# Optimization experiments

Hardware: AMD Instinct MI355X
Metric: run time of the kernel (lower is better)

## Reference

```python
import jax, jax.numpy as jnp
import numpy as np

HEADS = 16
TARGET_TOKENS = 128  # deterministic choice of image_tokens (original picks randomly from [729,128])


def _1d_sincos(embed_dim, pos):
    omega = np.arange(embed_dim // 2, dtype=np.float32)
    omega /= embed_dim / 2.0
    omega = 1.0 / 10000 ** omega
    out = np.einsum('m,d->md', pos.reshape(-1), omega)
    return np.concatenate([np.sin(out), np.cos(out)], axis=1)


def spatial_pos_embed(embed_dim, grid_size):
    d_sp = embed_dim // 4 * 3
    gh = np.arange(grid_size, dtype=np.float32)
    grid = np.stack(np.meshgrid(gh, gh), axis=0).reshape([2, 1, grid_size, grid_size])
    emb = np.concatenate([_1d_sincos(d_sp // 2, grid[0]), _1d_sincos(d_sp // 2, grid[1])], axis=1)
    emb = emb[np.newaxis]
    pad = np.zeros((1, emb.shape[1], embed_dim - d_sp), dtype=np.float32)
    return np.concatenate([pad, emb], axis=-1).reshape(1, grid_size * grid_size, embed_dim)


def setup_inputs() -> dict:
    key = jax.random.key(0)
    ks = jax.random.split(key, 4)
    B, P, C, H = 64, 729, 1152, 3584
    x = jax.random.normal(ks[0], (B, P, C), jnp.float32)
    w1 = jax.random.normal(ks[1], (C, H), jnp.float32) * (1.0 / np.sqrt(C))
    b1 = jnp.zeros((H,), jnp.float32)
    w2 = jax.random.normal(ks[2], (H, H), jnp.float32) * (1.0 / np.sqrt(H))
    b2 = jnp.zeros((H,), jnp.float32)
    spatial_pos = jnp.asarray(spatial_pos_embed(C, 27))
    return {'x': x, 'spatial_pos': spatial_pos, 'w1': w1, 'b1': b1,
            'w2': w2, 'b2': b2, 'local_num_frames': 1}


def _match_indices(metric, r):
    # ToMe bipartite soft matching: metric [B, T, d]
    metric = metric / jnp.linalg.norm(metric, axis=-1, keepdims=True)
    a, b = metric[:, ::2], metric[:, 1::2]
    scores = jnp.einsum('bic,bjc->bij', a, b)   # [B, Ta, Tb]
    node_max = scores.max(-1)
    node_idx = scores.argmax(-1)
    edge_idx = jnp.argsort(-node_max, axis=-1)
    unm_idx = edge_idx[:, r:]                    # kept src tokens
    src_idx = edge_idx[:, :r]                    # merged src tokens
    dst_idx = jnp.take_along_axis(node_idx, src_idx, axis=-1)
    return unm_idx, src_idx, dst_idx


def _merge_sum(x, unm_idx, src_idx, dst_idx):
    src, dst = x[:, ::2], x[:, 1::2]
    unm = jnp.take_along_axis(src, unm_idx[:, :, None], axis=1)
    sel = jnp.take_along_axis(src, src_idx[:, :, None], axis=1)
    dst = jax.vmap(lambda d, i, v: d.at[i].add(v))(dst, dst_idx, sel)
    return jnp.concatenate([unm, dst], axis=1)


def merge_tokens(x, target, heads):
    b, p, c = x.shape
    if p == target:
        return x
    rs, tmp = [], p
    while tmp != target:
        if tmp - target <= tmp // 2:
            rs.append(tmp - target)
            break
        rs.append(tmp // 2)
        tmp -= tmp // 2
    size = jnp.ones((b, p, 1), x.dtype)
    for r in rs:  # static schedule, e.g. [364, 182, 55]
        t = x.shape[1]
        metric = x.reshape(b, t, heads, c // heads).mean(2)
        idxs = _match_indices(metric, r)
        x = _merge_sum(x * size, *idxs)
        size = _merge_sum(size, *idxs)
        x = x / size
    return x


def reference(x, spatial_pos, w1, b1, w2, b2, local_num_frames):
    # is_image=True path
    x = x + spatial_pos
    x = merge_tokens(x, TARGET_TOKENS, HEADS)
    h = jax.nn.gelu(jnp.einsum('bpc,ch->bph', x, w1) + b1, approximate=False)
    return jnp.einsum('bph,ho->bpo', h, w2) + b2
```

## Files before the change

### kernel.cpp

```cpp
#include <hip/hip_runtime.h>
#include <hip/hip_bf16.h>
#include <stdint.h>

#define BB 64
#define P0 729
#define CC 1152
#define HD 72
#define NHEAD 16
#define HH 3584
#define TT 128
#define NSTR 365
#define SCB 384
#define MAXCB 6

typedef __hip_bfloat16 bf16;
typedef unsigned short u16;
typedef __attribute__((ext_vector_type(8))) short short8;
typedef __attribute__((ext_vector_type(4))) float floatx4;

__device__ inline u16 f2bf(float v) {
  bf16 h = __float2bfloat16(v);
  return *(u16*)&h;
}

__device__ inline void load_lds16(const void* g, void* l) {
  __builtin_amdgcn_global_load_lds(
      (const __attribute__((address_space(1))) uint32_t*)g,
      (__attribute__((address_space(3))) uint32_t*)l, 16, 0, 0);
}

__global__ __launch_bounds__(128)
void k_init(const float* __restrict__ x, const float* __restrict__ pos,
            double* __restrict__ mo, int* __restrict__ amap) {
  __shared__ float xs[CC], ps[CC];
  int bp = blockIdx.x;
  int p = bp % P0;
  int tid = threadIdx.x;
  const float4* xr = (const float4*)(x + (size_t)bp * CC);
  const float4* pr = (const float4*)(pos + (size_t)p * CC);
  for (int idx = tid; idx < CC / 4; idx += 128) {
    ((float4*)xs)[idx] = xr[idx];
    ((float4*)ps)[idx] = pr[idx];
  }
  __syncthreads();
  if (tid < HD) {
    double s = 0.0;
    #pragma unroll
    for (int h = 0; h < NHEAD; ++h) {
      int c = h * HD + tid;
      s += (double)xs[c] + (double)ps[c];
    }
    mo[(size_t)bp * HD + tid] = s * (1.0 / 16.0);
  }
  if (tid == 0) amap[bp] = p;
}

__global__ void k_rnorm(const double* __restrict__ m, double* __restrict__ rn, int t) {
  int bi = blockIdx.x;
  int lane = threadIdx.x;
  const double* row = m + (size_t)bi * HD;
  double v = 0.0;
  if (lane < HD) { double a = row[lane]; v = a * a; }
  if (lane < HD - 64) { double a = row[lane + 64]; v += a * a; }
  for (int off = 32; off; off >>= 1) v += __shfl_down(v, off, 64);
  if (lane == 0) {
    int b = bi / t, i = bi % t;
    rn[b * P0 + i] = 1.0 / sqrt(v);
  }
}

__global__ __launch_bounds__(256)
void k_score2(const double* __restrict__ m, const double* __restrict__ rn,
              double* __restrict__ pmax, int* __restrict__ pidx,
              int t, int s, int d) {
  __shared__ double sL[64][37];
  __shared__ double sD[64][37];
  int b = blockIdx.z;
  int i0 = blockIdx.x * 64, j0 = blockIdx.y * 64;
  int tid = threadIdx.x;
  int tx = tid & 15, ty = tid >> 4;
  double acc[4][4] = {};
  for (int kc = 0; kc < HD; kc += 36) {
    for (int idx = tid; idx < 64 * 36; idx += 256) {
      int row = idx / 36, k = idx - row * 36;
      int i = i0 + row;
      sL[row][k] = (i < s) ? m[((size_t)b * t + 2 * i) * HD + kc + k] : 0.0;
      int j = j0 + row;
      sD[row][k] = (j < d) ? m[((size_t)b * t + 2 * j + 1) * HD + kc + k] : 0.0;
    }
    __syncthreads();
    #pragma unroll 6
    for (int k = 0; k < 36; ++k) {
      double la[4], ld[4];
      #pragma unroll
      for (int a = 0; a < 4; ++a) la[a] = sL[ty + 16 * a][k];
      #pragma unroll
      for (int c = 0; c < 4; ++c) ld[c] = sD[tx + 16 * c][k];
      #pragma unroll
      for (int a = 0; a < 4; ++a)
        #pragma unroll
        for (int c = 0; c < 4; ++c)
          acc[a][c] += la[a] * ld[c];
    }
    __syncthreads();
  }
  #pragma unroll
  for (int a = 0; a < 4; ++a) {
    int i = i0 + ty + 16 * a;
    double rni = (i < s) ? rn[b * P0 + 2 * i] : 0.0;
    double best = -1e300; int bj = 0x7fffffff;
    #pragma unroll
    for (int c = 0; c < 4; ++c) {
      int j = j0 + tx + 16 * c;
      double sc = (j < d) ? acc[a][c] * rni * rn[b * P0 + 2 * j + 1] : -1e300;
      if (sc > best) { best = sc; bj = j; }
    }
    for (int off = 8; off; off >>= 1) {
      double ov = __shfl_down(best, off, 16);
      int oj = __shfl_down(bj, off, 16);
      if (ov > best || (ov == best && oj < bj)) { best = ov; bj = oj; }
    }
    if (tx == 0 && i < s) {
      pmax[((size_t)b * MAXCB + blockIdx.y) * SCB + i] = best;
      pidx[((size_t)b * MAXCB + blockIdx.y) * SCB + i] = bj;
    }
  }
}

__global__ void k_colred(const double* __restrict__ pmax, const int* __restrict__ pidx,
                         double* __restrict__ nmax, int* __restrict__ nidx,
                         int s, int ncb) {
  int b = blockIdx.x, i = threadIdx.x;
  if (i >= s) return;
  double best = -1e300; int bj = 0x7fffffff;
  for (int cb = 0; cb < ncb; ++cb) {
    double v = pmax[((size_t)b * MAXCB + cb) * SCB + i];
    int j = pidx[((size_t)b * MAXCB + cb) * SCB + i];
    if (v > best) { best = v; bj = j; }
  }
  nmax[b * NSTR + i] = best; nidx[b * NSTR + i] = bj;
}

template <int SZ>
__global__ __launch_bounds__(512)
void k_sort(const double* __restrict__ nmax, int* __restrict__ eidx, int s) {
  __shared__ double v[SZ];
  __shared__ int ix[SZ];
  int b = blockIdx.x, tid = threadIdx.x;
  if (tid < s) { v[tid] = nmax[b * NSTR + tid]; ix[tid] = tid; }
  else { v[tid] = -1e308; ix[tid] = 1024 + tid; }
  __syncthreads();
  for (int k = 2; k <= SZ; k <<= 1)
    for (int j = k >> 1; j > 0; j >>= 1) {
      int l = tid ^ j;
      if (l > tid) {
        double va = v[tid], vb = v[l]; int ia = ix[tid], ib = ix[l];
        bool b_before_a = (vb > va) || (vb == va && ib < ia);
        bool a_before_b = (va > vb) || (va == vb && ia < ib);
        bool dir = ((tid & k) == 0);
        bool sw = dir ? b_before_a : a_before_b;
        if (sw) { v[tid] = vb; v[l] = va; ix[tid] = ib; ix[l] = ia; }
      }
      __syncthreads();
    }
  if (tid < s) eidx[b * NSTR + tid] = ix[tid];
}

__global__ __launch_bounds__(512)
void k_mapround(const int* __restrict__ eidx, const int* __restrict__ nidx,
                int* __restrict__ amap, int t, int s, int r, int unm) {
  __shared__ int pos_of[NSTR];
  __shared__ int rmap[P0];
  int b = blockIdx.x, tid = threadIdx.x;
  for (int q = tid; q < s; q += 512) pos_of[eidx[b * NSTR + q]] = q;
  __syncthreads();
  for (int j = tid; j < t; j += 512) {
    int nm;
    if (j & 1) {
      nm = unm + (j >> 1);
    } else {
      int i = j >> 1;
      int q = pos_of[i];
      nm = (q >= r) ? (q - r)
                    : (unm + nidx[b * NSTR + i]);
    }
    rmap[j] = nm;
  }
  __syncthreads();
  for (int p = tid; p < P0; p += 512) {
    int cur = amap[b * P0 + p];
    amap[b * P0 + p] = rmap[cur];
  }
}

__global__ void k_gather_d(const double* __restrict__ mo, double* __restrict__ mn,
                           const int* __restrict__ eidx,
                           int t, int r, int unm, int tnew) {
  size_t idx = (size_t)blockIdx.x * 256 + threadIdx.x;
  size_t total = (size_t)BB * tnew * HD;
  if (idx >= total) return;
  int k = idx % HD;
  int o = (idx / HD) % tnew;
  int b = idx / ((size_t)HD * tnew);
  int tok = (o < unm) ? 2 * eidx[b * NSTR + r + o] : 2 * (o - unm) + 1;
  mn[idx] = mo[((size_t)b * t + tok) * HD + k];
}

__global__ void k_scatter_d(const double* __restrict__ mo, double* __restrict__ mn,
                            const int* __restrict__ eidx, const int* __restrict__ nidx,
                            int t, int r, int unm, int tnew) {
  size_t idx = (size_t)blockIdx.x * 256 + threadIdx.x;
  size_t total = (size_t)BB * r * HD;
  if (idx >= total) return;
  int k = idx % HD;
  int q = (idx / HD) % r;
  int b = idx / ((size_t)HD * r);
  int si = eidx[b * NSTR + q];
  int di = nidx[b * NSTR + si];
  atomicAdd(&mn[((size_t)b * tnew + unm + di) * HD + k],
            mo[((size_t)b * t + 2 * si) * HD + k]);
}

__global__ __launch_bounds__(256)
void k_buildcsr(const int* __restrict__ amap, int* __restrict__ sizes,
                int* __restrict__ offs, int* __restrict__ list) {
  __shared__ int cnt[TT], off_s[TT], cur[TT];
  int b = blockIdx.x, tid = threadIdx.x;
  if (tid < TT) { cnt[tid] = 0; cur[tid] = 0; }
  __syncthreads();
  for (int p = tid; p < P0; p += 256) atomicAdd(&cnt[amap[b * P0 + p]], 1);
  __syncthreads();
  if (tid == 0) {
    int acc = 0;
    for (int o = 0; o < TT; ++o) { off_s[o] = acc; acc += cnt[o]; }
  }
  __syncthreads();
  if (tid < TT) { sizes[b * TT + tid] = cnt[tid]; offs[b * TT + tid] = off_s[tid]; }
  for (int p = tid; p < P0; p += 256) {
    int o = amap[b * P0 + p];
    int pos = atomicAdd(&cur[o], 1);
    list[b * P0 + off_s[o] + pos] = p;
  }
}

__global__ __launch_bounds__(256)
void k_assemble(const float* __restrict__ x, const float* __restrict__ pos,
                const int* __restrict__ sizes, const int* __restrict__ offs,
                const int* __restrict__ list, bf16* __restrict__ xb) {
  __shared__ int ml[P0];
  int o = blockIdx.x, b = blockIdx.y, tid = threadIdx.x;
  int n = sizes[b * TT + o];
  int off = offs[b * TT + o];
  for (int i = tid; i < n; i += 256) ml[i] = list[b * P0 + off + i];
  __syncthreads();
  const int C4 = CC / 4;
  const bool two = (tid < C4 - 256);
  float4 a0 = {0.f, 0.f, 0.f, 0.f}, a1 = {0.f, 0.f, 0.f, 0.f};
  int i = 0;
  for (; i + 4 <= n; i += 4) {
    int p0 = ml[i], p1 = ml[i + 1], p2 = ml[i + 2], p3 = ml[i + 3];
    const float4* x0 = (const float4*)(x + ((size_t)b * P0 + p0) * CC);
    const float4* x1 = (const float4*)(x + ((size_t)b * P0 + p1) * CC);
    const float4* x2 = (const float4*)(x + ((size_t)b * P0 + p2) * CC);
    const float4* x3 = (const float4*)(x + ((size_t)b * P0 + p3) * CC);
    const float4* q0 = (const float4*)(pos + (size_t)p0 * CC);
    const float4* q1 = (const float4*)(pos + (size_t)p1 * CC);
    const float4* q2 = (const float4*)(pos + (size_t)p2 * CC);
    const float4* q3 = (const float4*)(pos + (size_t)p3 * CC);
    float4 v0 = x0[tid], v1 = x1[tid], v2 = x2[tid], v3 = x3[tid];
    float4 w0 = q0[tid], w1 = q1[tid], w2 = q2[tid], w3 = q3[tid];
    a0.x += (v0.x + w0.x) + (v1.x + w1.x) + (v2.x + w2.x) + (v3.x + w3.x);
    a0.y += (v0.y + w0.y) + (v1.y + w1.y) + (v2.y + w2.y) + (v3.y + w3.y);
    a0.z += (v0.z + w0.z) + (v1.z + w1.z) + (v2.z + w2.z) + (v3.z + w3.z);
    a0.w += (v0.w + w0.w) + (v1.w + w1.w) + (v2.w + w2.w) + (v3.w + w3.w);
    if (two) {
      float4 u0 = x0[tid + 256], u1 = x1[tid + 256], u2 = x2[tid + 256], u3 = x3[tid + 256];
      float4 s0 = q0[tid + 256], s1 = q1[tid + 256], s2 = q2[tid + 256], s3 = q3[tid + 256];
      a1.x += (u0.x + s0.x) + (u1.x + s1.x) + (u2.x + s2.x) + (u3.x + s3.x);
      a1.y += (u0.y + s0.y) + (u1.y + s1.y) + (u2.y + s2.y) + (u3.y + s3.y);
      a1.z += (u0.z + s0.z) + (u1.z + s1.z) + (u2.z + s2.z) + (u3.z + s3.z);
      a1.w += (u0.w + s0.w) + (u1.w + s1.w) + (u2.w + s2.w) + (u3.w + s3.w);
    }
  }
  for (; i < n; ++i) {
    int p = ml[i];
    const float4* xr = (const float4*)(x + ((size_t)b * P0 + p) * CC);
    const float4* pr = (const float4*)(pos + (size_t)p * CC);
    float4 v = xr[tid], w = pr[tid];
    a0.x += v.x + w.x; a0.y += v.y + w.y; a0.z += v.z + w.z; a0.w += v.w + w.w;
    if (two) {
      float4 v1 = xr[tid + 256], w1 = pr[tid + 256];
      a1.x += v1.x + w1.x; a1.y += v1.y + w1.y; a1.z += v1.z + w1.z; a1.w += v1.w + w1.w;
    }
  }
  float inv = 1.0f / (float)n;
  bf16* orow = xb + ((size_t)b * TT + o) * CC;
  ushort4 pk;
  pk.x = f2bf(a0.x * inv);
  pk.y = f2bf(a0.y * inv);
  pk.z = f2bf(a0.z * inv);
  pk.w = f2bf(a0.w * inv);
  ((ushort4*)orow)[tid] = pk;
  if (two) {
    ushort4 pk1;
    pk1.x = f2bf(a1.x * inv);
    pk1.y = f2bf(a1.y * inv);
    pk1.z = f2bf(a1.z * inv);
    pk1.w = f2bf(a1.w * inv);
    ((ushort4*)orow)[tid + 256] = pk1;
  }
}

__global__ void k_transpose(const float* __restrict__ w, bf16* __restrict__ wt,
                            int K, int N) {
  __shared__ float tile[32][33];
  int n0 = blockIdx.x * 32, k0 = blockIdx.y * 32;
  int tx = threadIdx.x, ty = threadIdx.y;
  #pragma unroll
  for (int yy = 0; yy < 32; yy += 8)
    tile[ty + yy][tx] = w[(size_t)(k0 + ty + yy) * N + n0 + tx];
  __syncthreads();
  #pragma unroll
  for (int yy = 0; yy < 32; yy += 8)
    wt[(size_t)(n0 + ty + yy) * K + k0 + tx] = __float2bfloat16(tile[tx][ty + yy]);
}


#define SBAR __builtin_amdgcn_sched_barrier(0)

#define STAGE_A(BUF, HHF, KT) do {                                        \
    int ktc_ = (KT) < nkt ? (KT) : nkt - 1;                               \
    const u16* s_ = gA + (size_t)(HHF) * 128 * K + ktc_ * 64;             \
    u16* d_ = dA + (BUF) * 16384 + (HHF) * 8192;                          \
    load_lds16(s_, d_);                                                   \
    load_lds16(s_ + (size_t)64 * K, d_ + 4096);                           \
  } while (0)

#define STAGE_B(BUF, HHF, KT) do {                                        \
    int ktc_ = (KT) < nkt ? (KT) : nkt - 1;                               \
    const u16* s_ = gB + (size_t)(HHF) * 128 * K + ktc_ * 64;             \
    u16* d_ = dB + (BUF) * 16384 + (HHF) * 8192;                          \
    load_lds16(s_, d_);                                                   \
    load_lds16(s_ + (size_t)64 * K, d_ + 4096);                           \
  } while (0)

#define LOADA(QA) do {                                                    \
    _Pragma("unroll")                                                     \
    for (int f_ = 0; f_ < 4; ++f_) {                                      \
      const u16* p_ = Ab + ((QA) * 128 + wr64 + f_ * 16 + lrow) * 64;     \
      af[f_][0] = *(const short8*)(p_ + swo0);                            \
      af[f_][1] = *(const short8*)(p_ + swo1);                            \
    }                                                                     \
  } while (0)

#define LOADB(QB) do {                                                    \
    _Pragma("unroll")                                                     \
    for (int g_ = 0; g_ < 2; ++g_) {                                      \
      const u16* p_ = Bb + ((QB) * 128 + wc32 + g_ * 16 + lrow) * 64;     \
      bfr[g_][0] = *(const short8*)(p_ + swo0);                           \
      bfr[g_][1] = *(const short8*)(p_ + swo1);                           \
    }                                                                     \
  } while (0)

#define DO_MFMA(QA, QB) do {                                              \
    _Pragma("unroll")                                                     \
    for (int ks_ = 0; ks_ < 2; ++ks_)                                     \
      _Pragma("unroll")                                                   \
      for (int f_ = 0; f_ < 4; ++f_)                                      \
        _Pragma("unroll")                                                 \
        for (int g_ = 0; g_ < 2; ++g_)                                    \
          acc[QA][QB][f_][g_] = __builtin_amdgcn_mfma_f32_16x16x32_bf16(  \
              af[f_][ks_], bfr[g_][ks_], acc[QA][QB][f_][g_], 0, 0, 0);   \
  } while (0)

#define MIDBAR() do {                                                     \
    SBAR;                                                                 \
    __builtin_amdgcn_s_barrier();                                         \
    asm volatile("s_waitcnt lgkmcnt(0)" ::: "memory");                    \
    SBAR;                                                                 \
    __builtin_amdgcn_s_setprio(1);                                        \
  } while (0)

#define ENDBAR() do {                                                     \
    __builtin_amdgcn_s_setprio(0);                                        \
    SBAR;                                                                 \
    __builtin_amdgcn_s_barrier();                                         \
    SBAR;                                                                 \
  } while (0)

#define ENDBAR_VM() do {                                                  \
    __builtin_amdgcn_s_setprio(0);                                        \
    SBAR;                                                                 \
    asm volatile("s_waitcnt vmcnt(6)" ::: "memory");                      \
    SBAR;                                                                 \
    __builtin_amdgcn_s_barrier();                                         \
    SBAR;                                                                 \
  } while (0)

template <int EPI>
__global__ __launch_bounds__(512, 2)
void k_gemm(const u16* __restrict__ A, const u16* __restrict__ Bt,
            const float* __restrict__ bias, void* __restrict__ Cout,
            int M, int N, int K) {
  __shared__ u16 sAall[32768];
  __shared__ u16 sBall[32768];
  (void)M;
  const int tid = threadIdx.x;
  const int m0 = blockIdx.y * 256, n0 = blockIdx.x * 256;
  const int wave = tid >> 6, lane = tid & 63;
  const int wr64 = (wave >> 2) * 64;
  const int wc32 = (wave & 3) * 32;
  const int quad = lane >> 4, lrow = lane & 15;
  const int sw = lrow & 7;
  const int swo0 = ((quad ^ sw)) << 3;
  const int swo1 = (((quad | 4) ^ sw)) << 3;
  const int nkt = K >> 6;

  const int r = tid >> 3;
  const int c16 = (tid & 7) ^ (r & 7);
  const u16* gA = A + (size_t)(m0 + r) * K + c16 * 8;
  const u16* gB = Bt + (size_t)(n0 + r) * K + c16 * 8;
  u16* dA = sAall + (tid << 3);
  u16* dB = sBall + (tid << 3);

  floatx4 acc[2][2][4][2] = {};
  short8 af[4][2], bfr[2][2];

  STAGE_A(0, 0, 0); STAGE_B(0, 1, 0); STAGE_A(0, 1, 0); STAGE_B(0, 0, 0);
  STAGE_A(1, 0, 1); STAGE_B(1, 1, 1); STAGE_A(1, 1, 1);
  SBAR;
  asm volatile("s_waitcnt vmcnt(6)" ::: "memory");
  SBAR;
  __builtin_amdgcn_s_barrier();
  SBAR;

  for (int t = 0; t < nkt; ++t) {
    const int bb = t & 1;
    const u16* Ab = sAall + bb * 16384;
    const u16* Bb = sBall + bb * 16384;
    LOADA(0); LOADB(0);
    STAGE_B(bb ^ 1, 0, t + 1);
    MIDBAR(); DO_MFMA(0, 0); ENDBAR();
    LOADB(1);
    STAGE_A(bb, 0, t + 2);
    MIDBAR(); DO_MFMA(0, 1); ENDBAR();
    LOADA(1);
    STAGE_B(bb, 1, t + 2);
    MIDBAR(); DO_MFMA(1, 1); ENDBAR();
    LOADB(0);
    STAGE_A(bb, 1, t + 2);
    MIDBAR(); DO_MFMA(1, 0); ENDBAR_VM();
  }

  #pragma unroll
  for (int qb = 0; qb < 2; ++qb)
    #pragma unroll
    for (int g = 0; g < 2; ++g) {
      int col = n0 + qb * 128 + wc32 + g * 16 + lrow;
      float bc = bias[col];
      #pragma unroll
      for (int qa = 0; qa < 2; ++qa)
        #pragma unroll
        for (int f = 0; f < 4; ++f)
          #pragma unroll
          for (int rg = 0; rg < 4; ++rg) {
            int row = m0 + qa * 128 + wr64 + f * 16 + quad * 4 + rg;
            float v = acc[qa][qb][f][g][rg] + bc;
            if (EPI == 0) {
              float gl = 0.5f * v * (1.0f + erff(v * 0.70710678118654752f));
              ((bf16*)Cout)[(size_t)row * N + col] = __float2bfloat16(gl);
            } else {
              ((float*)Cout)[(size_t)row * N + col] = v;
            }
          }
    }
}

extern "C" void kernel_launch(void* const* d_in, const int* in_sizes, int n_in,
                              void* d_out, int out_size, void* d_ws, size_t ws_size,
                              hipStream_t stream) {
  const float* x   = (const float*)d_in[0];
  const float* pos = (const float*)d_in[1];
  const float* w1  = (const float*)d_in[2];
  const float* b1  = (const float*)d_in[3];
  const float* w2  = (const float*)d_in[4];
  const float* b2  = (const float*)d_in[5];

  uint8_t* wsp = (uint8_t*)d_ws;
  size_t off = 0;
  auto alloc = [&](size_t bytes) -> void* {
    void* p = wsp + off;
    off += (bytes + 255) & ~(size_t)255;
    return p;
  };
  double* m_a  = (double*)alloc((size_t)BB * P0 * HD * 8);
  double* m_b  = (double*)alloc((size_t)BB * NSTR * HD * 8);
  double* rn   = (double*)alloc((size_t)BB * P0 * 8);
  double* nmax = (double*)alloc((size_t)BB * NSTR * 8);
  int*    nidx = (int*)alloc((size_t)BB * NSTR * 4);
  int*    eidx = (int*)alloc((size_t)BB * NSTR * 4);
  double* pmax = (double*)alloc((size_t)BB * MAXCB * SCB * 8);
  int*    pidx = (int*)alloc((size_t)BB * MAXCB * SCB * 4);
  int*    amap = (int*)alloc((size_t)BB * P0 * 4);
  int*    szs  = (int*)alloc((size_t)BB * TT * 4);
  int*    offs = (int*)alloc((size_t)BB * TT * 4);
  int*    list = (int*)alloc((size_t)BB * P0 * 4);
  bf16*   xb   = (bf16*)alloc((size_t)BB * TT * CC * 2);
  bf16*   w1t  = (bf16*)alloc((size_t)HH * CC * 2);
  bf16*   w2t  = (bf16*)alloc((size_t)HH * HH * 2);
  bf16*   hb   = (bf16*)alloc((size_t)BB * TT * HH * 2);

  k_init<<<BB * P0, 128, 0, stream>>>(x, pos, m_a, amap);
  dim3 tb(32, 8);
  k_transpose<<<dim3(HH / 32, CC / 32), tb, 0, stream>>>(w1, w1t, CC, HH);
  k_transpose<<<dim3(HH / 32, HH / 32), tb, 0, stream>>>(w2, w2t, HH, HH);

  struct Rnd { int t, s, d, r, unm, tnew; };
  const Rnd R[3] = {{729, 365, 364, 364, 1, 365},
                    {365, 183, 182, 182, 1, 183},
                    {183,  92,  91,  55, 37, 128}};
  double* msrc[3] = {m_a, m_b, m_a};
  double* mdst[3] = {m_b, m_a, m_b};

  for (int rr = 0; rr < 3; ++rr) {
    Rnd q = R[rr];
    k_rnorm<<<BB * q.t, 64, 0, stream>>>(msrc[rr], rn, q.t);
    int rt = (q.s + 63) / 64, ct = (q.d + 63) / 64;
    dim3 sg(rt, ct, BB);
    k_score2<<<sg, 256, 0, stream>>>(msrc[rr], rn, pmax, pidx, q.t, q.s, q.d);
    k_colred<<<BB, 512, 0, stream>>>(pmax, pidx, nmax, nidx, q.s, ct);
    if (rr == 0)      k_sort<512><<<BB, 512, 0, stream>>>(nmax, eidx, q.s);
    else if (rr == 1) k_sort<256><<<BB, 256, 0, stream>>>(nmax, eidx, q.s);
    else              k_sort<128><<<BB, 128, 0, stream>>>(nmax, eidx, q.s);
    k_mapround<<<BB, 512, 0, stream>>>(eidx, nidx, amap, q.t, q.s, q.r, q.unm);
    if (rr < 2) {
      size_t tg = (size_t)BB * q.tnew * HD;
      k_gather_d<<<(tg + 255) / 256, 256, 0, stream>>>(msrc[rr], mdst[rr], eidx, q.t, q.r, q.unm, q.tnew);
      size_t ts = (size_t)BB * q.r * HD;
      k_scatter_d<<<(ts + 255) / 256, 256, 0, stream>>>(msrc[rr], mdst[rr], eidx, nidx, q.t, q.r, q.unm, q.tnew);
    }
  }

  k_buildcsr<<<BB, 256, 0, stream>>>(amap, szs, offs, list);
  k_assemble<<<dim3(TT, BB), 256, 0, stream>>>(x, pos, szs, offs, list, xb);

  k_gemm<0><<<dim3(HH / 256, (BB * TT) / 256), 512, 0, stream>>>(
      (const u16*)xb, (const u16*)w1t, b1, hb, BB * TT, HH, CC);
  k_gemm<1><<<dim3(HH / 256, (BB * TT) / 256), 512, 0, stream>>>(
      (const u16*)hb, (const u16*)w2t, b2, d_out, BB * TT, HH, HH);
}
```

Before: 1.204 ms.

## Double-buffer MFMA fragments across phases and swizzle workgroups per XCD

The GEMM main loop now keeps two register sets for the A and B fragments. The next A fragment is prefetched from the other LDS buffer while the current phase's MFMAs run, and the lgkmcnt waits are relaxed to partial counts so LDS reads overlap compute. Workgroup IDs are also remapped so consecutive tiles land on the same XCD, which should improve L2 reuse. The extra fragment registers raise register pressure under the 512x2 launch bounds, and the reworked waits carry a risk of subtle ordering hazards.

Result: faster. 1.124 ms (-6.7%).

```diff
diff --git a/kernel.cpp b/kernel.cpp
--- a/kernel.cpp
+++ b/kernel.cpp
@@ -344,25 +344,25 @@
     load_lds16(s_ + (size_t)64 * K, d_ + 4096);                           \
   } while (0)
 
-#define LOADA(QA) do {                                                    \
+#define LOAD_A(DST, BUF, QA) do {                                        \
     _Pragma("unroll")                                                     \
     for (int f_ = 0; f_ < 4; ++f_) {                                      \
-      const u16* p_ = Ab + ((QA) * 128 + wr64 + f_ * 16 + lrow) * 64;     \
-      af[f_][0] = *(const short8*)(p_ + swo0);                            \
-      af[f_][1] = *(const short8*)(p_ + swo1);                            \
+      const u16* p_ = (BUF) + ((QA) * 128 + wr64 + f_ * 16 + lrow) * 64;  \
+      DST[f_][0] = *(const short8*)(p_ + swo0);                           \
+      DST[f_][1] = *(const short8*)(p_ + swo1);                           \
     }                                                                     \
   } while (0)
 
-#define LOADB(QB) do {                                                    \
+#define LOAD_B(DST, BUF, QB) do {                                        \
     _Pragma("unroll")                                                     \
     for (int g_ = 0; g_ < 2; ++g_) {                                      \
-      const u16* p_ = Bb + ((QB) * 128 + wc32 + g_ * 16 + lrow) * 64;     \
-      bfr[g_][0] = *(const short8*)(p_ + swo0);                           \
-      bfr[g_][1] = *(const short8*)(p_ + swo1);                           \
+      const u16* p_ = (BUF) + ((QB) * 128 + wc32 + g_ * 16 + lrow) * 64;  \
+      DST[g_][0] = *(const short8*)(p_ + swo0);                           \
+      DST[g_][1] = *(const short8*)(p_ + swo1);                           \
     }                                                                     \
   } while (0)
 
-#define DO_MFMA(QA, QB) do {                                              \
+#define DO_MFMA(AF, BF, QA, QB) do {                                      \
     _Pragma("unroll")                                                     \
     for (int ks_ = 0; ks_ < 2; ++ks_)                                     \
       _Pragma("unroll")                                                   \
@@ -370,32 +370,10 @@
         _Pragma("unroll")                                                 \
         for (int g_ = 0; g_ < 2; ++g_)                                    \
           acc[QA][QB][f_][g_] = __builtin_amdgcn_mfma_f32_16x16x32_bf16(  \
-              af[f_][ks_], bfr[g_][ks_], acc[QA][QB][f_][g_], 0, 0, 0);   \
+              AF[f_][ks_], BF[g_][ks_], acc[QA][QB][f_][g_], 0, 0, 0);    \
   } while (0)
 
-#define MIDBAR() do {                                                     \
-    SBAR;                                                                 \
-    __builtin_amdgcn_s_barrier();                                         \
-    asm volatile("s_waitcnt lgkmcnt(0)" ::: "memory");                    \
-    SBAR;                                                                 \
-    __builtin_amdgcn_s_setprio(1);                                        \
-  } while (0)
-
-#define ENDBAR() do {                                                     \
-    __builtin_amdgcn_s_setprio(0);                                        \
-    SBAR;                                                                 \
-    __builtin_amdgcn_s_barrier();                                         \
-    SBAR;                                                                 \
-  } while (0)
-
-#define ENDBAR_VM() do {                                                  \
-    __builtin_amdgcn_s_setprio(0);                                        \
-    SBAR;                                                                 \
-    asm volatile("s_waitcnt vmcnt(6)" ::: "memory");                      \
-    SBAR;                                                                 \
-    __builtin_amdgcn_s_barrier();                                         \
-    SBAR;                                                                 \
-  } while (0)
+#define PH_BAR() do { SBAR; __builtin_amdgcn_s_barrier(); SBAR; } while (0)
 
 template <int EPI>
 __global__ __launch_bounds__(512, 2)
@@ -406,7 +384,12 @@
   __shared__ u16 sBall[32768];
   (void)M;
   const int tid = threadIdx.x;
-  const int m0 = blockIdx.y * 256, n0 = blockIdx.x * 256;
+  const int nwg = gridDim.x * gridDim.y;
+  const int wg = blockIdx.y * gridDim.x + blockIdx.x;
+  const int qx = nwg >> 3, rx = nwg & 7;
+  const int xcd = wg & 7, loc = wg >> 3;
+  const int swz = (xcd < rx ? xcd * (qx + 1) : rx * (qx + 1) + (xcd - rx) * qx) + loc;
+  const int m0 = (swz / gridDim.x) * 256, n0 = (swz % gridDim.x) * 256;
   const int wave = tid >> 6, lane = tid & 63;
   const int wr64 = (wave >> 2) * 64;
   const int wc32 = (wave & 3) * 32;
@@ -424,7 +407,8 @@
   u16* dB = sBall + (tid << 3);
 
   floatx4 acc[2][2][4][2] = {};
-  short8 af[4][2], bfr[2][2];
+  short8 af0[4][2], af1[4][2];
+  short8 bf0[2][2], bf1[2][2];
 
   STAGE_A(0, 0, 0); STAGE_B(0, 1, 0); STAGE_A(0, 1, 0); STAGE_B(0, 0, 0);
   STAGE_A(1, 0, 1); STAGE_B(1, 1, 1); STAGE_A(1, 1, 1);
@@ -433,23 +417,50 @@
   SBAR;
   __builtin_amdgcn_s_barrier();
   SBAR;
+  LOAD_A(af0, sAall, 0);
 
   for (int t = 0; t < nkt; ++t) {
     const int bb = t & 1;
     const u16* Ab = sAall + bb * 16384;
     const u16* Bb = sBall + bb * 16384;
-    LOADA(0); LOADB(0);
+    const u16* Ao = sAall + (bb ^ 1) * 16384;
+    LOAD_B(bf0, Bb, 0);
+    LOAD_B(bf1, Bb, 1);
     STAGE_B(bb ^ 1, 0, t + 1);
-    MIDBAR(); DO_MFMA(0, 0); ENDBAR();
-    LOADB(1);
+    SBAR; __builtin_amdgcn_s_barrier();
+    asm volatile("s_waitcnt lgkmcnt(4)" ::: "memory");
+    SBAR;
+    __builtin_amdgcn_s_setprio(1);
+    DO_MFMA(af0, bf0, 0, 0);
+    __builtin_amdgcn_s_setprio(0);
+    PH_BAR();
+    LOAD_A(af1, Ab, 1);
     STAGE_A(bb, 0, t + 2);
-    MIDBAR(); DO_MFMA(0, 1); ENDBAR();
-    LOADA(1);
+    SBAR; __builtin_amdgcn_s_barrier();
+    asm volatile("s_waitcnt lgkmcnt(8)" ::: "memory");
+    SBAR;
+    __builtin_amdgcn_s_setprio(1);
+    DO_MFMA(af0, bf1, 0, 1);
+    __builtin_amdgcn_s_setprio(0);
+    PH_BAR();
     STAGE_B(bb, 1, t + 2);
-    MIDBAR(); DO_MFMA(1, 1); ENDBAR();
-    LOADB(0);
+    SBAR;
+    asm volatile("s_waitcnt vmcnt(4)" ::: "memory");
+    SBAR;
+    __builtin_amdgcn_s_barrier();
+    asm volatile("s_waitcnt lgkmcnt(0)" ::: "memory");
+    SBAR;
+    __builtin_amdgcn_s_setprio(1);
+    DO_MFMA(af1, bf1, 1, 1);
+    __builtin_amdgcn_s_setprio(0);
+    PH_BAR();
+    LOAD_A(af0, Ao, 0);
     STAGE_A(bb, 1, t + 2);
-    MIDBAR(); DO_MFMA(1, 0); ENDBAR_VM();
+    SBAR; __builtin_amdgcn_s_barrier(); SBAR;
+    __builtin_amdgcn_s_setprio(1);
+    DO_MFMA(af1, bf0, 1, 0);
+    __builtin_amdgcn_s_setprio(0);
+    PH_BAR();
   }
 
   #pragma unroll
```
